# Kernel tuning notes

Measured on AMD Instinct MI355X. Metric: run time of the kernel, lower is better.

Reference implementation:

```python
import jax, jax.numpy as jnp
import numpy as np

N_NODES = 30000
N_EDGES = 150000
N_GRAPHS = 64
TOWERS = 5
F_IN = 75
F_OUT = 15
STD_EPS = 1e-5
BN_EPS = 1e-5


def setup_inputs() -> dict:
    key = jax.random.key(0)
    ks = jax.random.split(key, 16)
    s = 0.05
    edge_index = jax.random.randint(ks[0], (2, N_EDGES), 0, N_NODES)
    deg = jnp.zeros(N_NODES, jnp.float32).at[edge_index[1]].add(1.0)
    u = jax.random.uniform(ks[1], (N_NODES, 1), jnp.float32, 1e-10, 1.0 - 1e-10)
    return {
        "x": jax.random.normal(ks[2], (N_NODES, 2), jnp.float32),
        "alpha": jax.random.uniform(ks[3], (N_GRAPHS,), jnp.float32),
        "edge_index": edge_index,
        "batch": jnp.sort(jax.random.randint(ks[4], (N_NODES,), 0, N_GRAPHS)),
        "noise": jnp.log(u) - jnp.log1p(-u),  # logistic (Gumbel-sigmoid) noise
        "avg_deg_log": jnp.log1p(deg).mean(),
        "pre_w": jax.random.normal(ks[5], (2, F_IN), jnp.float32) * s,
        "pre_b": jnp.zeros((F_IN,), jnp.float32),
        "W_pre": jax.random.normal(ks[6], (4, TOWERS, 2 * F_IN, F_IN), jnp.float32) * s,
        "b_pre": jnp.zeros((4, TOWERS, F_IN), jnp.float32),
        "W_post": jax.random.normal(ks[7], (4, TOWERS, 13 * F_IN, F_OUT), jnp.float32) * s,
        "b_post": jnp.zeros((4, TOWERS, F_OUT), jnp.float32),
        "W_lin": jax.random.normal(ks[8], (4, F_IN, F_IN), jnp.float32) * s,
        "b_lin": jnp.zeros((4, F_IN), jnp.float32),
        "bn_g": jnp.ones((4, F_IN), jnp.float32),
        "bn_b": jnp.zeros((4, F_IN), jnp.float32),
        "mw1": jax.random.normal(ks[9], (F_IN + 1, 50), jnp.float32) * s,
        "mb1": jnp.zeros((50,), jnp.float32),
        "mw2": jax.random.normal(ks[10], (50, 25), jnp.float32) * s,
        "mb2": jnp.zeros((25,), jnp.float32),
        "mw3": jax.random.normal(ks[11], (25, 1), jnp.float32) * s,
        "mb3": jnp.zeros((1,), jnp.float32),
    }


def _batchnorm(x, g, b):
    mu = x.mean(0)
    var = x.var(0)  # biased, matches torch BN normalization
    return g * (x - mu) * jax.lax.rsqrt(var + BN_EPS) + b


def _pna_layer(x, src, dst, deg, avg_deg_log, Wp, bp, Wq, bq, Wl, bl):
    n = x.shape[0]
    # message: per-tower pre MLP on cat([x_i, x_j]); x_i = target, x_j = source
    h = jnp.concatenate([x[dst], x[src]], axis=-1)  # [E, 150]
    m = jnp.einsum('ef,tfo->eto', h, Wp) + bp       # [E, T, F_IN]
    cnt = jnp.maximum(deg, 1.0)[:, None, None]
    has = (deg > 0)[:, None, None]
    mean = jax.ops.segment_sum(m, dst, num_segments=n) / cnt
    mean2 = jax.ops.segment_sum(m * m, dst, num_segments=n) / cnt
    std = jnp.sqrt(jax.nn.relu(mean2 - mean * mean) + STD_EPS)
    mn = jnp.where(has, jax.ops.segment_min(m, dst, num_segments=n), 0.0)
    mx = jnp.where(has, jax.ops.segment_max(m, dst, num_segments=n), 0.0)
    agg = jnp.concatenate([mean, mn, mx, std], axis=-1)  # [N, T, 4*F_IN]
    amp = jnp.log1p(jnp.maximum(deg, 1.0))[:, None, None] / avg_deg_log
    scaled = jnp.concatenate([agg, agg * amp, agg / amp], axis=-1)  # [N, T, 12*F_IN]
    xt = jnp.broadcast_to(x[:, None, :], (n, TOWERS, F_IN))
    out = jnp.concatenate([xt, scaled], axis=-1)  # [N, T, 13*F_IN]
    out = jnp.einsum('nti,tio->nto', out, Wq) + bq  # [N, T, F_OUT]
    out = out.reshape(n, TOWERS * F_OUT)
    return out @ Wl + bl


def _forward(x, alpha, edge_index, batch, noise, avg_deg_log, pre_w, pre_b,
             W_pre, b_pre, W_post, b_post, W_lin, b_lin, bn_g, bn_b,
             mw1, mb1, mw2, mb2, mw3, mb3):
    src, dst = edge_index[0], edge_index[1]
    deg = jnp.zeros(x.shape[0], x.dtype).at[dst].add(1.0)
    fixed_feature = x[:, 0:1]
    h = x @ pre_w + pre_b
    for l in range(4):
        h = _pna_layer(h, src, dst, deg, avg_deg_log, W_pre[l], b_pre[l],
                       W_post[l], b_post[l], W_lin[l], b_lin[l])
        h = jax.nn.relu(_batchnorm(h, bn_g[l], bn_b[l]))
    h = jnp.concatenate([h, alpha[batch][:, None]], axis=-1)  # [N, 76]
    h = jax.nn.relu(h @ mw1 + mb1)
    h = jax.nn.relu(h @ mw2 + mb2)
    h = h @ mw3 + mb3
    out = jax.nn.sigmoid(h + noise)
    return out, fixed_feature


def reference(x, alpha, edge_index, batch, noise, avg_deg_log, pre_w, pre_b,
              W_pre, b_pre, W_post, b_post, W_lin, b_lin, bn_g, bn_b,
              mw1, mb1, mw2, mb2, mw3, mb3):
    return _forward(x, alpha, edge_index, batch, noise, avg_deg_log, pre_w, pre_b,
                    W_pre, b_pre, W_post, b_post, W_lin, b_lin, bn_g, bn_b,
                    mw1, mb1, mw2, mb2, mw3, mb3)
```

## Files before the change

### kernel.cpp

```cpp
#include <hip/hip_runtime.h>
#include <hip/hip_bf16.h>
#include <cstdint>
#include <cstddef>

#define NN 30000
#define EE 150000
#define BASE_XS 120
#define LIN_XS 120

using u16 = unsigned short;
using u32 = unsigned int;

__device__ __forceinline__ float bl2f(u16 u) { return __uint_as_float(((u32)u) << 16); }
__device__ __forceinline__ u16 f2bl(float f) {
    u32 x = __float_as_uint(f);
    return (u16)((x + 0x7fffu + ((x >> 16) & 1u)) >> 16);
}
__device__ __forceinline__ u32 pack2(float a, float b) {
    return (u32)f2bl(a) | ((u32)f2bl(b) << 16);
}

__global__ void k_count(const int* __restrict__ dst, int* __restrict__ cnt) {
    int e = blockIdx.x * 256 + threadIdx.x;
    if (e < EE) atomicAdd(&cnt[dst[e]], 1);
}

__global__ void k_scan(const int* __restrict__ cnt, int* __restrict__ offs) {
    __shared__ int ss[1024];
    int t = threadIdx.x;
    int base = t * 30;
    int s = 0;
    for (int i = 0; i < 30; i++) { int idx = base + i; if (idx < NN) s += cnt[idx]; }
    ss[t] = s; __syncthreads();
    for (int off = 1; off < 1024; off <<= 1) {
        int v = (t >= off) ? ss[t - off] : 0;
        __syncthreads();
        ss[t] += v;
        __syncthreads();
    }
    int run = (t == 0) ? 0 : ss[t - 1];
    for (int i = 0; i < 30; i++) {
        int idx = base + i;
        if (idx < NN) { offs[idx] = run; run += cnt[idx]; }
    }
    if (t == 1023) offs[NN] = run;
}

__global__ void k_scatter(const int* __restrict__ src, const int* __restrict__ dst,
                          const int* __restrict__ offs, int* __restrict__ fill,
                          int* __restrict__ csr) {
    int e = blockIdx.x * 256 + threadIdx.x;
    if (e < EE) {
        int d = dst[e];
        int p = offs[d] + atomicAdd(&fill[d], 1);
        csr[p] = src[e];
    }
}

__global__ void k_wqt(const float* __restrict__ W_post, float* __restrict__ wqt) {
    int idx = blockIdx.x * 256 + threadIdx.x;
    if (idx >= 270000) return;
    int j = idx % 15;
    int grp = (idx / 15) % 3;
    int s4 = (idx / 45) % 4;
    int c = (idx / 180) % 75;
    int lt = idx / 13500;
    wqt[idx] = W_post[(size_t)lt * 975 * 15 + (size_t)(75 + grp * 300 + s4 * 75 + c) * 15 + j];
}

__global__ void k_badj(const float* __restrict__ b_lin, const float* __restrict__ b_post,
                       const float* __restrict__ W_lin, float* __restrict__ bladj) {
    int idx = blockIdx.x * 256 + threadIdx.x;
    if (idx >= 300) return;
    int l = idx / 75, c = idx % 75;
    float a = b_lin[l * 75 + c];
    const float* bq = b_post + l * 75;
    const float* Wl = W_lin + (size_t)l * 75 * 75;
    for (int k = 0; k < 75; k++) a = fmaf(bq[k], Wl[k * 75 + c], a);
    bladj[idx] = a;
}

__global__ void k_wm(const float* __restrict__ W_post, const float* __restrict__ W_lin,
                     float* __restrict__ Mf) {
    int idx = blockIdx.x * 256 + threadIdx.x;
    if (idx >= 22500) return;
    int l = idx / 5625;
    int c = (idx / 75) % 75;
    int o = idx % 75;
    const float* Wq = W_post + (size_t)l * 5 * 975 * 15;
    const float* Wl = W_lin + (size_t)l * 75 * 75;
    float a = 0.f;
    for (int t5 = 0; t5 < 5; t5++) {
        const float* wr = Wq + (size_t)t5 * 975 * 15 + (size_t)c * 15;
        const float* lr = Wl + (size_t)(t5 * 15) * 75 + o;
#pragma unroll
        for (int j = 0; j < 15; j++) a = fmaf(wr[j], lr[(size_t)j * 75], a);
    }
    Mf[idx] = a;
}

__global__ void k_pre(const float* __restrict__ x, const float* __restrict__ pw,
                      const float* __restrict__ pb, float* __restrict__ hT,
                      u32* __restrict__ hB) {
    int n = blockIdx.x * 256 + threadIdx.x;
    if (n >= NN) return;
    float x0 = x[2 * n], x1 = x[2 * n + 1];
    float buf[80];
#pragma unroll
    for (int c = 0; c < 80; c++)
        buf[c] = (c < 75) ? fmaf(x0, pw[c], fmaf(x1, pw[75 + c], pb[c])) : 0.f;
#pragma unroll
    for (int c = 0; c < 75; c++)
        hT[(size_t)c * NN + n] = buf[c];
    uint4* bp4 = (uint4*)(hB + (size_t)n * 40);
#pragma unroll
    for (int w = 0; w < 10; w++)
        bp4[w] = make_uint4(pack2(buf[8 * w], buf[8 * w + 1]), pack2(buf[8 * w + 2], buf[8 * w + 3]),
                            pack2(buf[8 * w + 4], buf[8 * w + 5]), pack2(buf[8 * w + 6], buf[8 * w + 7]));
}

__device__ __forceinline__ float upk(const uint4& a, int k) {
    u32 u = (k < 2) ? a.x : (k < 4) ? a.y : (k < 6) ? a.z : a.w;
    return __uint_as_float((k & 1) ? (u & 0xffff0000u) : (u << 16));
}

__device__ __forceinline__ void gemm30s(const uint4* __restrict__ h,
                                        const float* __restrict__ wA,
                                        const float* __restrict__ wB,
                                        float acc[30]) {
    for (int fq = 0; fq < 9; fq++) {
        uint4 a0 = h[fq];
#pragma unroll
        for (int k = 0; k < 8; k++) {
            float i0 = upk(a0, k);
            const float* ra = wA + (fq * 8 + k) * 75;
            const float* rb = wB + (fq * 8 + k) * 75;
#pragma unroll
            for (int j = 0; j < 15; j++) acc[j] = fmaf(i0, ra[j], acc[j]);
#pragma unroll
            for (int j = 0; j < 15; j++) acc[15 + j] = fmaf(i0, rb[j], acc[15 + j]);
        }
    }
    uint4 a0 = h[9];
#pragma unroll
    for (int k = 0; k < 3; k++) {
        float i0 = upk(a0, k);
        const float* ra = wA + (72 + k) * 75;
        const float* rb = wB + (72 + k) * 75;
#pragma unroll
        for (int j = 0; j < 15; j++) acc[j] = fmaf(i0, ra[j], acc[j]);
#pragma unroll
        for (int j = 0; j < 15; j++) acc[15 + j] = fmaf(i0, rb[j], acc[15 + j]);
    }
}

__device__ __forceinline__ void chunk_w(int p, const float* Wp, int half_off,
                                        const float** wA, const float** wB, bool* full) {
    int cg = p * 2;
    int tA = cg / 5, cA = (cg % 5) * 15;
    *full = p < 12;
    int cg1 = *full ? cg + 1 : cg;
    int tB = cg1 / 5, cB = (cg1 % 5) * 15;
    *wA = Wp + ((size_t)tA * 150 + half_off) * 75 + cA;
    *wB = Wp + ((size_t)tB * 150 + half_off) * 75 + cB;
}

__device__ __forceinline__ void pack_row(u32* rp, const float* a, bool full) {
    if (full) {
#pragma unroll
        for (int w = 0; w < 15; w++) rp[w] = pack2(a[2 * w], a[2 * w + 1]);
    } else {
#pragma unroll
        for (int w = 0; w < 7; w++) rp[w] = pack2(a[2 * w], a[2 * w + 1]);
        rp[7] = pack2(a[14], 0.f);
    }
}

__global__ __launch_bounds__(256) void k_base(const u32* __restrict__ hB,
                                              const float* __restrict__ Wp,
                                              const float* __restrict__ bp,
                                              u32* __restrict__ baseb32,
                                              u32* __restrict__ srcb32) {
    int b = blockIdx.x;
    int p = b / BASE_XS;
    int xx = b - p * BASE_XS;
    int n = xx * 256 + threadIdx.x;
    if (n >= NN) return;
    uint4 h[10];
    const uint4* hp = (const uint4*)(hB + (size_t)n * 40);
#pragma unroll
    for (int w = 0; w < 10; w++) h[w] = hp[w];
    int o0 = p * 30;
    {
        const float *wA, *wB; bool full;
        chunk_w(p, Wp, 0, &wA, &wB, &full);
        float acc[30];
#pragma unroll
        for (int j = 0; j < 15; j++) acc[j] = bp[o0 + j];
#pragma unroll
        for (int j = 0; j < 15; j++) acc[15 + j] = full ? bp[o0 + 15 + j] : 0.f;
        gemm30s(h, wA, wB, acc);
        pack_row(baseb32 + (size_t)n * 188 + p * 15, acc, full);
    }
    {
        const float *wA, *wB; bool full;
        chunk_w(p, Wp, 75, &wA, &wB, &full);
        float acc[30];
#pragma unroll
        for (int j = 0; j < 30; j++) acc[j] = 0.f;
        gemm30s(h, wA, wB, acc);
        pack_row(srcb32 + (size_t)n * 188 + p * 15, acc, full);
    }
}

__global__ __launch_bounds__(192) void k_agg(const u32* __restrict__ srcb32,
                                             const int* __restrict__ csr,
                                             const int* __restrict__ offs,
                                             const u32* __restrict__ baseb32,
                                             u32* __restrict__ agg32) {
    int q = threadIdx.x;
    if (q >= 188) return;
    int o0 = 2 * q, o1 = 2 * q + 1;
    bool has1 = o1 < 375;
    int t0 = o0 / 75, c0 = o0 % 75;
    int t1 = has1 ? (o1 / 75) : 0, c1 = has1 ? (o1 % 75) : 0;
    int z0 = (c0 >= 40) ? 1 : 0;
    size_t fb0 = (size_t)(t0 * 2 + z0) * NN * 80;
    int a0o = z0 ? (c0 - 40) : c0;
    int b0o = z0 ? (c0 - 4) : (40 + c0);
    int z1 = (c1 >= 40) ? 1 : 0;
    size_t fb1 = (size_t)(t1 * 2 + z1) * NN * 80;
    int a1o = z1 ? (c1 - 40) : c1;
    int b1o = z1 ? (c1 - 4) : (40 + c1);
    for (int v = blockIdx.x; v < NN; v += gridDim.x) {
        int e0 = offs[v], e1 = offs[v + 1];
        float s0 = 0.f, s1 = 0.f, sq0 = 0.f, sq1 = 0.f;
        float mn0 = 3.4e38f, mn1 = 3.4e38f, mx0 = -3.4e38f, mx1 = -3.4e38f;
        for (int e = e0; e < e1; e++) {
            int s = csr[e];
            u32 w = srcb32[(size_t)s * 188 + q];
            float x0 = bl2f((u16)(w & 0xffffu)), x1 = bl2f((u16)(w >> 16));
            s0 += x0; sq0 = fmaf(x0, x0, sq0); mn0 = fminf(mn0, x0); mx0 = fmaxf(mx0, x0);
            s1 += x1; sq1 = fmaf(x1, x1, sq1); mn1 = fminf(mn1, x1); mx1 = fmaxf(mx1, x1);
        }
        int deg = e1 - e0;
        u32 bw = baseb32[(size_t)v * 188 + q];
        float b0 = bl2f((u16)(bw & 0xffffu)), b1 = bl2f((u16)(bw >> 16));
        float mean0, mean1, mnf0, mnf1, mxf0, mxf1, sd0, sd1;
        if (deg > 0) {
            float im = 1.f / (float)deg;
            float mm0 = s0 * im, mm1 = s1 * im;
            float v0 = fmaxf(fmaf(-mm0, mm0, sq0 * im), 0.f);
            float v1 = fmaxf(fmaf(-mm1, mm1, sq1 * im), 0.f);
            sd0 = sqrtf(v0 + 1e-5f); sd1 = sqrtf(v1 + 1e-5f);
            mean0 = b0 + mm0; mean1 = b1 + mm1;
            mnf0 = b0 + mn0;  mnf1 = b1 + mn1;
            mxf0 = b0 + mx0;  mxf1 = b1 + mx1;
        } else {
            float sde = sqrtf(1e-5f);
            mean0 = mean1 = mnf0 = mnf1 = mxf0 = mxf1 = 0.f;
            sd0 = sd1 = sde;
        }
        u32* fp0 = agg32 + fb0 + (size_t)v * 80;
        fp0[a0o] = pack2(mean0, mnf0);
        fp0[b0o] = pack2(mxf0, sd0);
        if (has1) {
            u32* fp1 = agg32 + fb1 + (size_t)v * 80;
            fp1[a1o] = pack2(mean1, mnf1);
            fp1[b1o] = pack2(mxf1, sd1);
        }
    }
}

__device__ __forceinline__ void post_cq(int cq, uint4 A, uint4 B, float amp, float inv,
                                        const float* __restrict__ wq, float acc[15]) {
#pragma unroll
    for (int i = 0; i < 4; i++) {
        int c = cq * 4 + i;
        if (c < 75) {
            u32 wA = (i == 0) ? A.x : (i == 1) ? A.y : (i == 2) ? A.z : A.w;
            u32 wB = (i == 0) ? B.x : (i == 1) ? B.y : (i == 2) ? B.z : B.w;
            float vs[4];
            vs[0] = bl2f((u16)(wA & 0xffffu)); vs[1] = bl2f((u16)(wA >> 16));
            vs[2] = bl2f((u16)(wB & 0xffffu)); vs[3] = bl2f((u16)(wB >> 16));
            const float* wc = wq + c * 180;
#pragma unroll
            for (int s4 = 0; s4 < 4; s4++) {
                float a = vs[s4], aa = a * amp, ai = a * inv;
                const float* wb = wc + s4 * 45;
#pragma unroll
                for (int j = 0; j < 15; j++)
                    acc[j] = fmaf(a, wb[j], fmaf(aa, wb[15 + j], fmaf(ai, wb[30 + j], acc[j])));
            }
        }
    }
}

__global__ __launch_bounds__(256) void k_post(const int* __restrict__ offs,
                                              const u32* __restrict__ agg32,
                                              const float* __restrict__ wqt_l,
                                              const float* __restrict__ adl_p,
                                              float* __restrict__ tmp0,
                                              float* __restrict__ tmp1) {
    int t = blockIdx.y;
    int zz = blockIdx.z;
    int n = blockIdx.x * 256 + threadIdx.x;
    if (n >= NN) return;
    float adl = adl_p[0];
    int deg = offs[n + 1] - offs[n];
    float dc = (float)(deg > 0 ? deg : 1);
    float amp = log1pf(dc) / adl;
    float inv = 1.f / amp;
    const float* wq = wqt_l + (size_t)t * 13500;
    const uint4* ap = (const uint4*)(agg32 + ((size_t)(t * 2 + zz) * NN + n) * 80);
    float acc[15];
#pragma unroll
    for (int j = 0; j < 15; j++) acc[j] = 0.f;
    if (zz == 0) {
        uint4 A[10], B[10];
#pragma unroll
        for (int g = 0; g < 10; g++) { A[g] = ap[g]; B[g] = ap[10 + g]; }
#pragma unroll
        for (int g = 0; g < 10; g++) post_cq(g, A[g], B[g], amp, inv, wq, acc);
#pragma unroll
        for (int j = 0; j < 15; j++) tmp0[(size_t)(t * 15 + j) * NN + n] = acc[j];
    } else {
        uint4 A[9], B[9];
#pragma unroll
        for (int g = 0; g < 9; g++) { A[g] = ap[g]; B[g] = ap[9 + g]; }
#pragma unroll
        for (int g = 0; g < 9; g++) post_cq(10 + g, A[g], B[g], amp, inv, wq, acc);
#pragma unroll
        for (int j = 0; j < 15; j++) tmp1[(size_t)(t * 15 + j) * NN + n] = acc[j];
    }
}

__global__ __launch_bounds__(256) void k_lin2(const float* __restrict__ tmp0,
                                              const float* __restrict__ tmp1,
                                              const float* __restrict__ hT,
                                              const float* __restrict__ Wl,
                                              const float* __restrict__ Mf_l,
                                              const float* __restrict__ bladj,
                                              float* __restrict__ zF,
                                              float* __restrict__ bsum,
                                              float* __restrict__ bsq) {
    __shared__ __align__(16) float wl[75][16];
    __shared__ __align__(16) float wm[75][16];
    __shared__ float red1[4][15], red2[4][15];
    int b = blockIdx.x;
    int p = b / LIN_XS;
    int x = b - p * LIN_XS;
    for (int idx = threadIdx.x; idx < 75 * 15; idx += 256) {
        int k = idx / 15, j = idx % 15;
        wl[k][j] = Wl[k * 75 + p * 15 + j];
        wm[k][j] = Mf_l[k * 75 + p * 15 + j];
    }
    __syncthreads();
    int n = x * 256 + threadIdx.x;
    bool valid = n < NN;
    int nc = valid ? n : NN - 1;
    float acc[15];
#pragma unroll
    for (int j = 0; j < 15; j++) acc[j] = bladj[p * 15 + j];
    for (int k = 0; k < 75; k++) {
        float a = tmp0[(size_t)k * NN + nc] + tmp1[(size_t)k * NN + nc];
        float h = hT[(size_t)k * NN + nc];
        float4 w0 = *(const float4*)&wl[k][0];
        float4 w1 = *(const float4*)&wl[k][4];
        float4 w2 = *(const float4*)&wl[k][8];
        float4 w3 = *(const float4*)&wl[k][12];
        float4 m0 = *(const float4*)&wm[k][0];
        float4 m1 = *(const float4*)&wm[k][4];
        float4 m2 = *(const float4*)&wm[k][8];
        float4 m3 = *(const float4*)&wm[k][12];
        acc[0]  = fmaf(h, m0.x, fmaf(a, w0.x, acc[0]));
        acc[1]  = fmaf(h, m0.y, fmaf(a, w0.y, acc[1]));
        acc[2]  = fmaf(h, m0.z, fmaf(a, w0.z, acc[2]));
        acc[3]  = fmaf(h, m0.w, fmaf(a, w0.w, acc[3]));
        acc[4]  = fmaf(h, m1.x, fmaf(a, w1.x, acc[4]));
        acc[5]  = fmaf(h, m1.y, fmaf(a, w1.y, acc[5]));
        acc[6]  = fmaf(h, m1.z, fmaf(a, w1.z, acc[6]));
        acc[7]  = fmaf(h, m1.w, fmaf(a, w1.w, acc[7]));
        acc[8]  = fmaf(h, m2.x, fmaf(a, w2.x, acc[8]));
        acc[9]  = fmaf(h, m2.y, fmaf(a, w2.y, acc[9]));
        acc[10] = fmaf(h, m2.z, fmaf(a, w2.z, acc[10]));
        acc[11] = fmaf(h, m2.w, fmaf(a, w2.w, acc[11]));
        acc[12] = fmaf(h, m3.x, fmaf(a, w3.x, acc[12]));
        acc[13] = fmaf(h, m3.y, fmaf(a, w3.y, acc[13]));
        acc[14] = fmaf(h, m3.z, fmaf(a, w3.z, acc[14]));
    }
    if (valid) {
#pragma unroll
        for (int j = 0; j < 15; j++)
            zF[(size_t)(p * 15 + j) * NN + n] = acc[j];
    }
    float s[15], ss[15];
#pragma unroll
    for (int i = 0; i < 15; i++) {
        float a = valid ? acc[i] : 0.f;
        s[i] = a; ss[i] = a * a;
    }
    for (int d = 32; d > 0; d >>= 1) {
#pragma unroll
        for (int i = 0; i < 15; i++) {
            s[i] += __shfl_down(s[i], d);
            ss[i] += __shfl_down(ss[i], d);
        }
    }
    int wave = threadIdx.x >> 6, lane = threadIdx.x & 63;
    if (lane == 0) {
#pragma unroll
        for (int i = 0; i < 15; i++) { red1[wave][i] = s[i]; red2[wave][i] = ss[i]; }
    }
    __syncthreads();
    if (threadIdx.x < 15) {
        int i = threadIdx.x;
        float a = red1[0][i] + red1[1][i] + red1[2][i] + red1[3][i];
        float b2 = red2[0][i] + red2[1][i] + red2[2][i] + red2[3][i];
        atomicAdd(&bsum[p * 15 + i], a);
        atomicAdd(&bsq[p * 15 + i], b2);
    }
}

__global__ __launch_bounds__(256) void k_bn2(const float* __restrict__ zF,
                                             const float* __restrict__ bsum,
                                             const float* __restrict__ bsq,
                                             const float* __restrict__ g,
                                             const float* __restrict__ b,
                                             float* __restrict__ hT,
                                             u32* __restrict__ hB) {
    int n = blockIdx.x * 256 + threadIdx.x;
    if (n >= NN) return;
    float buf[80];
    for (int c = 0; c < 75; c++) {
        float mu = bsum[c] * (1.f / NN);
        float var = bsq[c] * (1.f / NN) - mu * mu;
        float sc = g[c] * rsqrtf(var + 1e-5f);
        float v = (zF[(size_t)c * NN + n] - mu) * sc + b[c];
        float r = v > 0.f ? v : 0.f;
        buf[c] = r;
        hT[(size_t)c * NN + n] = r;
    }
#pragma unroll
    for (int c = 75; c < 80; c++) buf[c] = 0.f;
    uint4* bp4 = (uint4*)(hB + (size_t)n * 40);
#pragma unroll
    for (int w = 0; w < 10; w++)
        bp4[w] = make_uint4(pack2(buf[8 * w], buf[8 * w + 1]), pack2(buf[8 * w + 2], buf[8 * w + 3]),
                            pack2(buf[8 * w + 4], buf[8 * w + 5]), pack2(buf[8 * w + 6], buf[8 * w + 7]));
}

__global__ __launch_bounds__(256) void k_mlp1(const float* __restrict__ hT,
                                              const float* __restrict__ alpha,
                                              const int* __restrict__ batch,
                                              const float* __restrict__ w1,
                                              const float* __restrict__ b1,
                                              float* __restrict__ t1) {
    int n = blockIdx.x * 256 + threadIdx.x;
    if (n >= NN) return;
    float acc[50];
#pragma unroll
    for (int j = 0; j < 50; j++) acc[j] = b1[j];
    for (int k = 0; k < 75; k++) {
        float in = hT[(size_t)k * NN + n];
        const float* wr = w1 + k * 50;
#pragma unroll
        for (int j = 0; j < 50; j++) acc[j] = fmaf(in, wr[j], acc[j]);
    }
    float a = alpha[batch[n]];
    const float* wr = w1 + 75 * 50;
#pragma unroll
    for (int j = 0; j < 50; j++) {
        float v = fmaf(a, wr[j], acc[j]);
        t1[(size_t)j * NN + n] = v > 0.f ? v : 0.f;
    }
}

__global__ void k_mlp2(const float* __restrict__ t1, const float* __restrict__ w2,
                       const float* __restrict__ b2, const float* __restrict__ w3,
                       const float* __restrict__ b3, const float* __restrict__ noise,
                       const float* __restrict__ x, float* __restrict__ out) {
    int n = blockIdx.x * 256 + threadIdx.x;
    if (n >= NN) return;
    float tr[50];
#pragma unroll
    for (int k = 0; k < 50; k++) tr[k] = t1[(size_t)k * NN + n];
    float y = b3[0];
#pragma unroll
    for (int k2 = 0; k2 < 25; k2++) {
        float acc = b2[k2];
#pragma unroll
        for (int k = 0; k < 50; k++) acc = fmaf(tr[k], w2[k * 25 + k2], acc);
        acc = acc > 0.f ? acc : 0.f;
        y = fmaf(acc, w3[k2], y);
    }
    float z = y + noise[n];
    float s = 1.f / (1.f + expf(-z));
    out[n] = s;
    out[NN + n] = x[2 * n];
}

extern "C" void kernel_launch(void* const* d_in, const int* in_sizes, int n_in,
                              void* d_out, int out_size, void* d_ws, size_t ws_size,
                              hipStream_t stream) {
    const float* x      = (const float*)d_in[0];
    const float* alpha  = (const float*)d_in[1];
    const int*   ei     = (const int*)d_in[2];
    const int*   batch  = (const int*)d_in[3];
    const float* noise  = (const float*)d_in[4];
    const float* adl    = (const float*)d_in[5];
    const float* pre_w  = (const float*)d_in[6];
    const float* pre_b  = (const float*)d_in[7];
    const float* W_pre  = (const float*)d_in[8];
    const float* b_pre  = (const float*)d_in[9];
    const float* W_post = (const float*)d_in[10];
    const float* b_post = (const float*)d_in[11];
    const float* W_lin  = (const float*)d_in[12];
    const float* b_lin  = (const float*)d_in[13];
    const float* bn_g   = (const float*)d_in[14];
    const float* bn_b   = (const float*)d_in[15];
    const float* mw1    = (const float*)d_in[16];
    const float* mb1    = (const float*)d_in[17];
    const float* mw2    = (const float*)d_in[18];
    const float* mb2    = (const float*)d_in[19];
    const float* mw3    = (const float*)d_in[20];
    const float* mb3    = (const float*)d_in[21];
    (void)in_sizes; (void)n_in; (void)out_size; (void)ws_size;

    char* ws = (char*)d_ws;
    size_t off = 0;
    auto alloc = [&](size_t bytes) -> char* {
        char* p = ws + off;
        off += (bytes + 255) & ~((size_t)255);
        return p;
    };
    float* hT     = (float*)alloc((size_t)75 * NN * 4);
    u32*   hB     = (u32*)alloc((size_t)NN * 40 * 4);
    float* zF     = (float*)alloc((size_t)75 * NN * 4);
    float* tmp0   = (float*)alloc((size_t)75 * NN * 4);
    float* tmp1   = (float*)alloc((size_t)75 * NN * 4);
    u32*   agg32  = (u32*)alloc((size_t)10 * NN * 80 * 4);
    u32*   baseb32= (u32*)alloc((size_t)NN * 188 * 4);
    u32*   srcb32 = (u32*)alloc((size_t)NN * 188 * 4);
    float* wqt    = (float*)alloc((size_t)270000 * 4);
    float* Mf     = (float*)alloc((size_t)22500 * 4);
    float* bladj  = (float*)alloc(300 * 4);
    int*   cnt    = (int*)alloc((size_t)NN * 4);
    int*   offs   = (int*)alloc((size_t)(NN + 1) * 4);
    int*   fill   = (int*)alloc((size_t)NN * 4);
    int*   csr    = (int*)alloc((size_t)EE * 4);
    float* bnsum  = (float*)alloc(4 * 75 * 4);
    float* bnsq   = (float*)alloc(4 * 75 * 4);

    hipMemsetAsync(cnt, 0, (size_t)NN * 4, stream);
    hipMemsetAsync(fill, 0, (size_t)NN * 4, stream);
    hipMemsetAsync(bnsum, 0, 4 * 75 * 4, stream);
    hipMemsetAsync(bnsq, 0, 4 * 75 * 4, stream);

    const int* src = ei;
    const int* dst = ei + EE;
    int eb = (EE + 255) / 256;
    int nb = (NN + 255) / 256;

    k_count<<<eb, 256, 0, stream>>>(dst, cnt);
    k_scan<<<1, 1024, 0, stream>>>(cnt, offs);
    k_scatter<<<eb, 256, 0, stream>>>(src, dst, offs, fill, csr);
    k_pre<<<nb, 256, 0, stream>>>(x, pre_w, pre_b, hT, hB);
    k_wqt<<<(270000 + 255) / 256, 256, 0, stream>>>(W_post, wqt);
    k_badj<<<2, 256, 0, stream>>>(b_lin, b_post, W_lin, bladj);
    k_wm<<<(22500 + 255) / 256, 256, 0, stream>>>(W_post, W_lin, Mf);

    for (int l = 0; l < 4; l++) {
        const float* Wp  = W_pre + (size_t)l * 5 * 150 * 75;
        const float* bp  = b_pre + l * 375;
        const float* wqtl= wqt + (size_t)l * 67500;
        const float* Wl  = W_lin + l * 75 * 75;
        k_base<<<13 * BASE_XS, 256, 0, stream>>>(hB, Wp, bp, baseb32, srcb32);
        k_agg<<<4096, 192, 0, stream>>>(srcb32, csr, offs, baseb32, agg32);
        k_post<<<dim3(nb, 5, 2), 256, 0, stream>>>(offs, agg32, wqtl, adl, tmp0, tmp1);
        k_lin2<<<5 * LIN_XS, 256, 0, stream>>>(tmp0, tmp1, hT, Wl, Mf + l * 5625,
                                               bladj + l * 75, zF,
                                               bnsum + l * 75, bnsq + l * 75);
        k_bn2<<<nb, 256, 0, stream>>>(zF, bnsum + l * 75, bnsq + l * 75,
                                      bn_g + l * 75, bn_b + l * 75, hT, hB);
    }

    float* t1 = tmp0;
    k_mlp1<<<nb, 256, 0, stream>>>(hT, alpha, batch, mw1, mb1, t1);
    k_mlp2<<<nb, 256, 0, stream>>>(t1, mw2, mb2, mw3, mb3, noise, x, (float*)d_out);
}
```

Measured before the change: 1.421 ms.

## Store per-tower base/source projections in chunked 16-word slots with vector writes

The base and source projection buffers change from row-major [N,188] words to a chunk-major [13][N][16] layout. Each k_base thread now writes its chunk as four aligned 16-byte stores, and neighbouring threads write neighbouring slots, so the old strided per-word row writes become coalesced. k_agg is rewritten to index this layout, but each gathered source row is now split across 13 separate 64-byte segments. That likely touches more cache lines per edge in the gather, which may offset the cheaper writes.

```diff
diff --git a/kernel.cpp b/kernel.cpp
--- a/kernel.cpp
+++ b/kernel.cpp
@@ -165,15 +165,24 @@
     *wB = Wp + ((size_t)tB * 150 + half_off) * 75 + cB;
 }
 
-__device__ __forceinline__ void pack_row(u32* rp, const float* a, bool full) {
+__device__ __forceinline__ void pack_row16(u32* rp, const float* a, bool full) {
+    u32 t[16];
     if (full) {
 #pragma unroll
-        for (int w = 0; w < 15; w++) rp[w] = pack2(a[2 * w], a[2 * w + 1]);
+        for (int w = 0; w < 15; w++) t[w] = pack2(a[2 * w], a[2 * w + 1]);
     } else {
 #pragma unroll
-        for (int w = 0; w < 7; w++) rp[w] = pack2(a[2 * w], a[2 * w + 1]);
-        rp[7] = pack2(a[14], 0.f);
-    }
+        for (int w = 0; w < 7; w++) t[w] = pack2(a[2 * w], a[2 * w + 1]);
+        t[7] = pack2(a[14], 0.f);
+#pragma unroll
+        for (int w = 8; w < 15; w++) t[w] = 0u;
+    }
+    t[15] = 0u;
+    uint4* q = (uint4*)rp;
+    q[0] = make_uint4(t[0], t[1], t[2], t[3]);
+    q[1] = make_uint4(t[4], t[5], t[6], t[7]);
+    q[2] = make_uint4(t[8], t[9], t[10], t[11]);
+    q[3] = make_uint4(t[12], t[13], t[14], t[15]);
 }
 
 __global__ __launch_bounds__(256) void k_base(const u32* __restrict__ hB,
@@ -191,6 +200,7 @@
 #pragma unroll
     for (int w = 0; w < 10; w++) h[w] = hp[w];
     int o0 = p * 30;
+    size_t slot = ((size_t)p * NN + n) * 16;
     {
         const float *wA, *wB; bool full;
         chunk_w(p, Wp, 0, &wA, &wB, &full);
@@ -200,7 +210,7 @@
 #pragma unroll
         for (int j = 0; j < 15; j++) acc[15 + j] = full ? bp[o0 + 15 + j] : 0.f;
         gemm30s(h, wA, wB, acc);
-        pack_row(baseb32 + (size_t)n * 188 + p * 15, acc, full);
+        pack_row16(baseb32 + slot, acc, full);
     }
     {
         const float *wA, *wB; bool full;
@@ -209,7 +219,7 @@
 #pragma unroll
         for (int j = 0; j < 30; j++) acc[j] = 0.f;
         gemm30s(h, wA, wB, acc);
-        pack_row(srcb32 + (size_t)n * 188 + p * 15, acc, full);
+        pack_row16(srcb32 + slot, acc, full);
     }
 }
 
@@ -220,6 +230,10 @@
                                              u32* __restrict__ agg32) {
     int q = threadIdx.x;
     if (q >= 188) return;
+    int pp = (q < 180) ? (q / 15) : 12;
+    int ww = (q < 180) ? (q % 15) : (q - 180);
+    const u32* sp = srcb32 + (size_t)pp * NN * 16 + ww;
+    const u32* bpp = baseb32 + (size_t)pp * NN * 16 + ww;
     int o0 = 2 * q, o1 = 2 * q + 1;
     bool has1 = o1 < 375;
     int t0 = o0 / 75, c0 = o0 % 75;
@@ -238,13 +252,13 @@
         float mn0 = 3.4e38f, mn1 = 3.4e38f, mx0 = -3.4e38f, mx1 = -3.4e38f;
         for (int e = e0; e < e1; e++) {
             int s = csr[e];
-            u32 w = srcb32[(size_t)s * 188 + q];
+            u32 w = sp[(size_t)s * 16];
             float x0 = bl2f((u16)(w & 0xffffu)), x1 = bl2f((u16)(w >> 16));
             s0 += x0; sq0 = fmaf(x0, x0, sq0); mn0 = fminf(mn0, x0); mx0 = fmaxf(mx0, x0);
             s1 += x1; sq1 = fmaf(x1, x1, sq1); mn1 = fminf(mn1, x1); mx1 = fmaxf(mx1, x1);
         }
         int deg = e1 - e0;
-        u32 bw = baseb32[(size_t)v * 188 + q];
+        u32 bw = bpp[(size_t)v * 16];
         float b0 = bl2f((u16)(bw & 0xffffu)), b1 = bl2f((u16)(bw >> 16));
         float mean0, mean1, mnf0, mnf1, mxf0, mxf1, sd0, sd1;
         if (deg > 0) {
@@ -540,8 +554,8 @@
     float* tmp0   = (float*)alloc((size_t)75 * NN * 4);
     float* tmp1   = (float*)alloc((size_t)75 * NN * 4);
     u32*   agg32  = (u32*)alloc((size_t)10 * NN * 80 * 4);
-    u32*   baseb32= (u32*)alloc((size_t)NN * 188 * 4);
-    u32*   srcb32 = (u32*)alloc((size_t)NN * 188 * 4);
+    u32*   baseb32= (u32*)alloc((size_t)13 * NN * 16 * 4);
+    u32*   srcb32 = (u32*)alloc((size_t)13 * NN * 16 * 4);
     float* wqt    = (float*)alloc((size_t)270000 * 4);
     float* Mf     = (float*)alloc((size_t)22500 * 4);
     float* bladj  = (float*)alloc(300 * 4);
```

Result: slower. 1.453 ms (+2.3%).
